# Kernel optimization log

Measured on AMD Instinct MI355X. Metric: run time of the kernel, lower is better.

Reference implementation:

```python
import jax, jax.numpy as jnp
import numpy as np

H = 256  # hidden_size
E = 768  # embedding dim / lstm input size
V = 7987 # vocab
B = 256  # batch
T = 512  # seq len


def setup_inputs() -> dict:
    key = jax.random.key(0)
    ks = jax.random.split(key, 12)
    s = 0.05
    return {
        "input_tensor": jax.random.randint(ks[0], (B, T), 0, V),
        "target_idx": jax.random.randint(ks[1], (B,), 0, T),
        "max_length": T,
        "emb": jax.random.normal(ks[2], (V, E), dtype=jnp.float32),
        "w_ih_f": jax.random.normal(ks[3], (4 * H, E), dtype=jnp.float32) * s,
        "w_hh_f": jax.random.normal(ks[4], (4 * H, H), dtype=jnp.float32) * s,
        "b_ih_f": jax.random.normal(ks[5], (4 * H,), dtype=jnp.float32) * s,
        "b_hh_f": jax.random.normal(ks[6], (4 * H,), dtype=jnp.float32) * s,
        "w_ih_b": jax.random.normal(ks[7], (4 * H, E), dtype=jnp.float32) * s,
        "w_hh_b": jax.random.normal(ks[8], (4 * H, H), dtype=jnp.float32) * s,
        "b_ih_b": jax.random.normal(ks[9], (4 * H,), dtype=jnp.float32) * s,
        "b_hh_b": jax.random.normal(ks[10], (4 * H,), dtype=jnp.float32) * s,
        "w_out": jax.random.normal(ks[11], (1, 2 * H), dtype=jnp.float32) * s,
        "b_out": jnp.zeros((1,), dtype=jnp.float32),
    }


def _lstm_cell(x, h, c, w_ih, w_hh, b):
    # PyTorch gate order: i, f, g, o
    gates = x @ w_ih.T + h @ w_hh.T + b  # [B, 4H]
    i, f, g, o = jnp.split(gates, 4, axis=-1)
    c_new = jax.nn.sigmoid(f) * c + jax.nn.sigmoid(i) * jnp.tanh(g)
    h_new = jax.nn.sigmoid(o) * jnp.tanh(c_new)
    return h_new, c_new


def reference(input_tensor, target_idx, max_length, emb,
              w_ih_f, w_hh_f, b_ih_f, b_hh_f,
              w_ih_b, w_hh_b, b_ih_b, b_hh_b,
              w_out, b_out):
    bsz = input_tensor.shape[0]
    # embed whole sequence up front: [T, B, E]
    xs = jnp.transpose(emb[input_tensor], (1, 0, 2))
    bf = b_ih_f + b_hh_f
    bb = b_ih_b + b_hh_b
    h0 = jnp.zeros((bsz, H), dtype=xs.dtype)
    init = (h0, h0, h0, h0)

    # NOTE: original calls bidirectional LSTM one step at a time carrying state,
    # so BOTH directions run forward in time (backward dir just uses reverse weights).
    def step(carry, x):
        hf, cf, hb, cb = carry
        hf, cf = _lstm_cell(x, hf, cf, w_ih_f, w_hh_f, bf)
        hb, cb = _lstm_cell(x, hb, cb, w_ih_b, w_hh_b, bb)
        return (hf, cf, hb, cb), jnp.concatenate([hf, hb], axis=-1)

    _, encoder_outputs = jax.lax.scan(step, init, xs)  # [T, B, 2H]
    # gather hidden state at each example's target index
    gathered = encoder_outputs[target_idx, jnp.arange(bsz)]  # [B, 2H]
    out = jax.nn.sigmoid(gathered @ w_out.T + b_out)  # [B, 1]
    return out[:, None, :]  # [B, 1, 1] matching torch output shape
```

## Files before the change

kernel.cpp:

```cpp
#include <hip/hip_runtime.h>
#include <hip/hip_bf16.h>

#define Bx 256
#define Tx 512
#define Ex 768
#define Hx 256
#define Gx 1024
#define Vx 7987

typedef unsigned short u16;
typedef unsigned int u32;
typedef __bf16 bf16;
typedef bf16 bf16x8 __attribute__((ext_vector_type(8)));
typedef u16 u16x8 __attribute__((ext_vector_type(8)));
typedef float f32x4 __attribute__((ext_vector_type(4)));
typedef int i32x4 __attribute__((ext_vector_type(4)));

__device__ __forceinline__ u16 f2bf(float f) {
  union { float f; u32 u; } x; x.f = f;
  u32 r = x.u + 0x7fffu + ((x.u >> 16) & 1u);
  return (u16)(r >> 16);
}
__device__ __forceinline__ float bf2f(u16 b) {
  union { u32 u; float f; } x; x.u = ((u32)b) << 16;
  return x.f;
}
__device__ __forceinline__ void gload16(const void* g, void* l) {
  __builtin_amdgcn_global_load_lds((const __attribute__((address_space(1))) u32*)g,
                                   (__attribute__((address_space(3))) u32*)l, 16, 0, 0);
}
__device__ __forceinline__ float sigf(float x) {
  return __builtin_amdgcn_rcpf(1.f + __builtin_amdgcn_exp2f(x * -1.442695041f));
}
__device__ __forceinline__ void bar_ds() {
  __builtin_amdgcn_sched_barrier(0);
  asm volatile("s_waitcnt lgkmcnt(0)" ::: "memory");
  __builtin_amdgcn_s_barrier();
  __builtin_amdgcn_sched_barrier(0);
}
#define WAITV(N) { asm volatile("s_waitcnt vmcnt(" #N ")"); __builtin_amdgcn_sched_barrier(0); }

__device__ __forceinline__ void gld8u(u16x8& d, const u16* base, u32 voff) {
  asm volatile("global_load_dwordx4 %0, %1, %2" : "=&v"(d) : "v"(voff), "s"(base));
}
__device__ __forceinline__ void mfma_i8(i32x4& d, i32x4 a, i32x4 b) {
  asm volatile("v_mfma_i32_16x16x64_i8 %0, %1, %2, %0" : "+v"(d) : "v"(a), "a"(b));
}


__global__ void k_cvt(const float* __restrict__ src, u16* __restrict__ dst, int n) {
  int i = blockIdx.x * blockDim.x + threadIdx.x;
  int st = gridDim.x * blockDim.x;
  for (; i < n; i += st) dst[i] = f2bf(src[i]);
}

__global__ void k_bias(const float* __restrict__ bihf, const float* __restrict__ bhhf,
                       const float* __restrict__ bihb, const float* __restrict__ bhhb,
                       float* __restrict__ bcat) {
  int i = blockIdx.x * blockDim.x + threadIdx.x;
  if (i < Gx) { bcat[i] = bihf[i] + bhhf[i]; bcat[Gx + i] = bihb[i] + bhhb[i]; }
}

__global__ void k_scales(const float* __restrict__ wf, const float* __restrict__ wb,
                         float* __restrict__ s) {
  int row = blockIdx.x;
  const float* w = (row < Gx) ? (wf + (size_t)row * Hx) : (wb + (size_t)(row - Gx) * Hx);
  int l = threadIdx.x;
  float m = 0.f;
  for (int j = l; j < Hx; j += 64) m = fmaxf(m, fabsf(w[j]));
#pragma unroll
  for (int off = 32; off; off >>= 1) m = fmaxf(m, __shfl_down(m, off));
  if (l == 0) s[row] = fmaxf(m, 1e-20f) * (1.f / 127.f);
}

__global__ void k_pack_i8(const float* __restrict__ wf, const float* __restrict__ wb,
                          const float* __restrict__ s, char* __restrict__ pk) {
  int i = blockIdx.x * 256 + threadIdx.x;
  int lane = i & 63, nb = (i >> 6) & 63, kc = (i >> 12) & 3, dir = (i >> 14) & 1;
  int n = nb * 16 + (lane & 15);
  int k0 = kc * 64 + ((lane >> 4) << 4);
  const float* w = dir ? wb : wf;
  float inv = 1.f / s[dir * Gx + n];
  int dw[4];
#pragma unroll
  for (int d4 = 0; d4 < 4; ++d4) {
    int v = 0;
#pragma unroll
    for (int j = 0; j < 4; ++j) {
      int q = (int)rintf(w[(size_t)n * Hx + k0 + d4 * 4 + j] * inv);
      v |= (q & 255) << (8 * j);
    }
    dw[d4] = v;
  }
  *(int4*)(pk + (size_t)i * 16) = make_int4(dw[0], dw[1], dw[2], dw[3]);
}

__global__ __launch_bounds__(256) void k_vproj(
    const u16* __restrict__ embbf, const u16* __restrict__ wih,
    const float* __restrict__ bcat, u16* __restrict__ vp) {
  __shared__ u16 sA[128 * 64];
  __shared__ u16 sB[128 * 64];
  const int tid = threadIdx.x;
  const int l = tid & 63, w = tid >> 6;
  const int bx = blockIdx.x & 15, by = blockIdx.x >> 4;
  const int wm = w >> 1, wn = w & 1;
  const int lr = l >> 3, lc = l & 7;

  f32x4 acc[4][4];
#pragma unroll
  for (int a = 0; a < 4; ++a)
#pragma unroll
    for (int b = 0; b < 4; ++b) acc[a][b] = f32x4{0.f, 0.f, 0.f, 0.f};

  size_t asrc[4], bsrc[4];
#pragma unroll
  for (int j = 0; j < 4; ++j) {
    int row = j * 32 + w * 8 + lr;
    int m = by * 128 + row;
    int er = (m < Vx) ? m : 0;
    asrc[j] = (size_t)er * (Ex * 2) + (size_t)((lc * 16) ^ ((row & 7) << 4));
    bsrc[j] = (size_t)(bx * 128 + row) * (Ex * 2) + (size_t)((lc * 16) ^ ((row & 7) << 4));
  }

  for (int kt = 0; kt < 12; ++kt) {
    const char* ebase = (const char*)embbf + (size_t)kt * 128;
    const char* wbase = (const char*)wih + (size_t)kt * 128;
#pragma unroll
    for (int j = 0; j < 4; ++j) {
      gload16(ebase + asrc[j], (char*)sA + (j * 32 + w * 8) * 128);
      gload16(wbase + bsrc[j], (char*)sB + (j * 32 + w * 8) * 128);
    }
    __syncthreads();
#pragma unroll
    for (int kk = 0; kk < 2; ++kk) {
      int kb = kk * 64 + ((l >> 4) * 16);
      bf16x8 av[4], bv[4];
#pragma unroll
      for (int f = 0; f < 4; ++f) {
        int r = wm * 64 + f * 16 + (l & 15);
        av[f] = *(const bf16x8*)((const char*)sA + r * 128 + (kb ^ ((r & 7) << 4)));
      }
#pragma unroll
      for (int f = 0; f < 4; ++f) {
        int n = wn * 64 + f * 16 + (l & 15);
        bv[f] = *(const bf16x8*)((const char*)sB + n * 128 + (kb ^ ((n & 7) << 4)));
      }
#pragma unroll
      for (int fm = 0; fm < 4; ++fm)
#pragma unroll
        for (int fn = 0; fn < 4; ++fn)
          acc[fm][fn] = __builtin_amdgcn_mfma_f32_16x16x32_bf16(av[fm], bv[fn], acc[fm][fn], 0, 0, 0);
    }
    __syncthreads();
  }
#pragma unroll
  for (int fn = 0; fn < 4; ++fn) {
    int col = bx * 128 + wn * 64 + fn * 16 + (l & 15);
    int dirc = col >> 10, c10 = col & 1023;
    int gq = c10 >> 8, wq = (c10 >> 5) & 7, fcq = (c10 >> 4) & 1, uq = c10 & 15;
    int pos = (wq * 16 + uq) * 8 + gq * 2 + fcq;
    float bias = bcat[col];
#pragma unroll
    for (int fm = 0; fm < 4; ++fm) {
      int m0 = by * 128 + wm * 64 + fm * 16 + ((l >> 4) << 2);
#pragma unroll
      for (int r = 0; r < 4; ++r)
        vp[((size_t)(m0 + r) * 2 + dirc) * 1024 + pos] = f2bf(acc[fm][fn][r] + bias);
    }
  }
}

#define STEPI(T, RB, WB, XC) {                                                \
  i32x4 acc[8];                                                               \
  _Pragma("unroll") for (int nt = 0; nt < 8; ++nt) acc[nt] = i32x4{0, 0, 0, 0}; \
  _Pragma("unroll") for (int kc = 0; kc < 4; ++kc) {                          \
    i32x4 a = *(const i32x4*)((RB) + kc * 1024 + aoff);                       \
    _Pragma("unroll") for (int nt = 0; nt < 8; ++nt)                          \
      mfma_i8(acc[nt], a, wres[kc][nt]);                                      \
  }                                                                           \
  asm volatile("s_nop 7\n\ts_nop 7");                                         \
  float ga[2][4];                                                             \
  _Pragma("unroll") for (int fc = 0; fc < 2; ++fc)                            \
    _Pragma("unroll") for (int g = 0; g < 4; ++g)                             \
      ga[fc][g] = (float)acc[g * 2 + fc][0] * qs[g * 2 + fc]                  \
                  + bf2f(XC[g * 2 + fc]);                                     \
  _Pragma("unroll") for (int fc = 0; fc < 2; ++fc) {                          \
    float si = sigf(ga[fc][0]);                                               \
    float sf = sigf(ga[fc][1]);                                               \
    float tv = 2.f * sigf(2.f * ga[fc][2]) - 1.f;                             \
    float so = sigf(ga[fc][3]);                                               \
    float cn = sf * creg[fc] + si * tv;                                       \
    float hn = so * (2.f * sigf(2.f * cn) - 1.f);                             \
    creg[fc] = cn;                                                            \
    if ((T) == tgt)                                                           \
      gath[(size_t)(b0 + q) * 512 + dir * 256 + w * 32 + fc * 16 + c] = hn;   \
    int qh = (int)rintf(hn * 127.f);                                          \
    _Pragma("unroll") for (int m = 0; m < 4; ++m)                             \
      *((WB) + wb_base + fc * 256 + m * 64 + (((q - m) & 3) << 4)) = (char)qh; \
  }                                                                           \
  bar_ds();                                                                   \
}

__global__ __launch_bounds__(512, 2) void k_rnn(
    const char* __restrict__ wq, const float* __restrict__ wsc,
    const u16* __restrict__ vp, const int* __restrict__ input,
    const int* __restrict__ target, float* __restrict__ gath) {
  __shared__ __align__(16) char shd[2][4096];
  __shared__ int stok[2048];
  const int tid = threadIdx.x;
  const int l = tid & 63, w = tid >> 6;
  const int q = l >> 4, c = l & 15;
  const int dir = blockIdx.x >> 6, slice = blockIdx.x & 63;
  const int b0 = slice * 4;
  const char* wqd = wq + (size_t)dir * 262144;

  i32x4 wres[4][8];
#pragma unroll
  for (int kc = 0; kc < 4; ++kc)
#pragma unroll
    for (int nt = 0; nt < 8; ++nt) {
      int nb = (nt >> 1) * 16 + w * 2 + (nt & 1);
      wres[kc][nt] = *(const i32x4*)(wqd + ((size_t)(kc * 64 + nb) * 64 + l) * 16);
    }
  float qs[8];
#pragma unroll
  for (int nt = 0; nt < 8; ++nt)
    qs[nt] = wsc[dir * Gx + (nt >> 1) * 256 + w * 32 + (nt & 1) * 16 + c] * (1.f / 127.f);

  for (int i = tid; i < 2048; i += 512)
    stok[i] = input[(b0 + (i >> 9)) * Tx + (i & 511)];
  for (int i = tid; i < 2048; i += 512) ((int*)shd)[i] = 0;

  float creg[2] = {0.f, 0.f};
  const int tgt = target[b0 + q];
  const u32 go2 = (u32)((w * 16 + c) * 16 + dir * 2048);
  const int tk0 = input[(b0 + q) * Tx + 0];
  const int tk1 = input[(b0 + q) * Tx + 1];

  const int aoff = (q << 8) + (c << 4);
  const int wb_base = (w >> 1) * 1024 + (w & 1) * 512 + c;
  const char* rb0 = &shd[0][0];
  const char* rb1 = &shd[1][0];
  char* wb0 = &shd[0][0];
  char* wb1 = &shd[1][0];

  __syncthreads();
  asm volatile("s_waitcnt vmcnt(0)" ::: "memory");
  __builtin_amdgcn_sched_barrier(0);

  u16x8 xvA, xvB;
  gld8u(xvA, vp, (u32)tk0 * 4096 + go2);
  gld8u(xvB, vp, (u32)tk1 * 4096 + go2);

#pragma unroll 1
  for (int t = 0; t < Tx; t += 2) {
    WAITV(0);
    u16x8 xcA = xvA, xcB = xvB;
    int ta = stok[q * 512 + ((t + 2 < Tx) ? t + 2 : Tx - 1)];
    int tb = stok[q * 512 + ((t + 3 < Tx) ? t + 3 : Tx - 1)];
    gld8u(xvA, vp, (u32)ta * 4096 + go2);
    gld8u(xvB, vp, (u32)tb * 4096 + go2);
    STEPI(t, rb0, wb1, xcA);
    STEPI(t + 1, rb1, wb0, xcB);
  }
}

__global__ void k_out(const float* __restrict__ gath, const float* __restrict__ wout,
                      const float* __restrict__ bout, float* __restrict__ out) {
  int b = blockIdx.x, l = threadIdx.x;
  float s = 0.f;
  for (int j = l; j < 512; j += 64) s += gath[(size_t)b * 512 + j] * wout[j];
#pragma unroll
  for (int off = 32; off; off >>= 1) s += __shfl_down(s, off);
  if (l == 0) out[b] = 1.f / (1.f + __expf(-(s + bout[0])));
}

extern "C" void kernel_launch(void* const* d_in, const int* in_sizes, int n_in,
                              void* d_out, int out_size, void* d_ws, size_t ws_size,
                              hipStream_t stream) {
  const int* input = (const int*)d_in[0];
  const int* target = (const int*)d_in[1];
  const float* emb  = (const float*)d_in[3];
  const float* wihf = (const float*)d_in[4];
  const float* whhf = (const float*)d_in[5];
  const float* bihf = (const float*)d_in[6];
  const float* bhhf = (const float*)d_in[7];
  const float* wihb = (const float*)d_in[8];
  const float* whhb = (const float*)d_in[9];
  const float* bihb = (const float*)d_in[10];
  const float* bhhb = (const float*)d_in[11];
  const float* wout = (const float*)d_in[12];
  const float* bout = (const float*)d_in[13];
  float* out = (float*)d_out;

  char* ws = (char*)d_ws;
  u16* embbf  = (u16*)(ws + 0);
  u16* wih    = (u16*)(ws + 12268032);
  char* wq    = (char*)(ws + 15413760);
  float* wsc  = (float*)(ws + 15938048);
  float* bcat = (float*)(ws + 15946240);
  float* gath = (float*)(ws + 15954432);
  u16* vp     = (u16*)(ws + 16478720);

  k_cvt<<<1024, 256, 0, stream>>>(emb, embbf, Vx * Ex);
  k_cvt<<<512, 256, 0, stream>>>(wihf, wih, Gx * Ex);
  k_cvt<<<512, 256, 0, stream>>>(wihb, wih + Gx * Ex, Gx * Ex);
  k_bias<<<4, 256, 0, stream>>>(bihf, bhhf, bihb, bhhb, bcat);
  k_scales<<<2048, 64, 0, stream>>>(whhf, whhb, wsc);
  k_pack_i8<<<128, 256, 0, stream>>>(whhf, whhb, wsc, wq);
  k_vproj<<<1008, 256, 0, stream>>>(embbf, wih, bcat, vp);
  k_rnn<<<128, 512, 0, stream>>>(wq, wsc, vp, input, target, gath);
  k_out<<<256, 64, 0, stream>>>(gath, wout, bout, out);
}
```

Before: 589.3 us.

## Quantize vocab input projections to int8 and halve batch per recurrent block

Measured after the change: 651.2 us. +10.5%, slower.

```diff
diff --git a/kernel.cpp b/kernel.cpp
--- a/kernel.cpp
+++ b/kernel.cpp
@@ -40,8 +40,8 @@
 }
 #define WAITV(N) { asm volatile("s_waitcnt vmcnt(" #N ")"); __builtin_amdgcn_sched_barrier(0); }
 
-__device__ __forceinline__ void gld8u(u16x8& d, const u16* base, u32 voff) {
-  asm volatile("global_load_dwordx4 %0, %1, %2" : "=&v"(d) : "v"(voff), "s"(base));
+__device__ __forceinline__ void gld2(int2& d, const char* base, u32 voff) {
+  asm volatile("global_load_dwordx2 %0, %1, %2" : "=&v"(d) : "v"(voff), "s"(base));
 }
 __device__ __forceinline__ void mfma_i8(i32x4& d, i32x4 a, i32x4 b) {
   asm volatile("v_mfma_i32_16x16x64_i8 %0, %1, %2, %0" : "+v"(d) : "v"(a), "a"(b));
@@ -170,7 +170,44 @@
   }
 }
 
-#define STEPI(T, RB, WB, XC) {                                                \
+__global__ __launch_bounds__(512) void k_vq(u16* __restrict__ vp, float* __restrict__ scg) {
+  const int tid = threadIdx.x;
+  const int l = tid & 63;
+  int row = blockIdx.x * 8 + (tid >> 6);
+  bool valid = row < 2 * Vx;
+  int rr = valid ? row : 2 * Vx - 1;
+  const u16* src = vp + (size_t)rr * 1024;
+  float v[16];
+  float m = 0.f;
+#pragma unroll
+  for (int j = 0; j < 16; ++j) {
+    v[j] = bf2f(src[l * 16 + j]);
+    m = fmaxf(m, fabsf(v[j]));
+  }
+#pragma unroll
+  for (int off = 32; off; off >>= 1) m = fmaxf(m, __shfl_xor(m, off));
+  float sc = fmaxf(m, 1e-20f) * (1.f / 127.f);
+  float inv = 1.f / sc;
+  if (valid && l == 0) scg[row] = sc;
+  __syncthreads();
+  if (valid) {
+    int dw[4];
+#pragma unroll
+    for (int d4 = 0; d4 < 4; ++d4) {
+      int wv = 0;
+#pragma unroll
+      for (int j = 0; j < 4; ++j) {
+        int qv = (int)rintf(v[d4 * 4 + j] * inv);
+        wv |= (qv & 255) << (8 * j);
+      }
+      dw[d4] = wv;
+    }
+    char* dst = (char*)vp + (size_t)blockIdx.x * 16384 + (size_t)(row & 7) * 1024;
+    *(int4*)(dst + l * 16) = make_int4(dw[0], dw[1], dw[2], dw[3]);
+  }
+}
+
+#define STEPI(T, RB, WB, XC, SC) {                                            \
   i32x4 acc[8];                                                               \
   _Pragma("unroll") for (int nt = 0; nt < 8; ++nt) acc[nt] = i32x4{0, 0, 0, 0}; \
   _Pragma("unroll") for (int kc = 0; kc < 4; ++kc) {                          \
@@ -181,9 +218,12 @@
   asm volatile("s_nop 7\n\ts_nop 7");                                         \
   float ga[2][4];                                                             \
   _Pragma("unroll") for (int fc = 0; fc < 2; ++fc)                            \
-    _Pragma("unroll") for (int g = 0; g < 4; ++g)                             \
-      ga[fc][g] = (float)acc[g * 2 + fc][0] * qs[g * 2 + fc]                  \
-                  + bf2f(XC[g * 2 + fc]);                                     \
+    _Pragma("unroll") for (int g = 0; g < 4; ++g) {                           \
+      int j = g * 2 + fc;                                                     \
+      int wd = (j < 4) ? (XC).x : (XC).y;                                     \
+      float xval = (float)((wd << (24 - 8 * (j & 3))) >> 24) * (SC);          \
+      ga[fc][g] = (float)acc[j][0] * qs[j] + xval;                            \
+    }                                                                         \
   _Pragma("unroll") for (int fc = 0; fc < 2; ++fc) {                          \
     float si = sigf(ga[fc][0]);                                               \
     float sf = sigf(ga[fc][1]);                                               \
@@ -192,26 +232,28 @@
     float cn = sf * creg[fc] + si * tv;                                       \
     float hn = so * (2.f * sigf(2.f * cn) - 1.f);                             \
     creg[fc] = cn;                                                            \
-    if ((T) == tgt)                                                           \
-      gath[(size_t)(b0 + q) * 512 + dir * 256 + w * 32 + fc * 16 + c] = hn;   \
+    if ((T) == tgt && q < 2)                                                  \
+      gath[(size_t)(b0 + (q & 1)) * 512 + dir * 256 + w * 32 + fc * 16 + c] = hn; \
     int qh = (int)rintf(hn * 127.f);                                          \
     _Pragma("unroll") for (int m = 0; m < 4; ++m)                             \
-      *((WB) + wb_base + fc * 256 + m * 64 + (((q - m) & 3) << 4)) = (char)qh; \
+      *((WB) + wb_base + fc * 256 + m * 16) = (char)qh;                       \
   }                                                                           \
   bar_ds();                                                                   \
 }
 
 __global__ __launch_bounds__(512, 2) void k_rnn(
     const char* __restrict__ wq, const float* __restrict__ wsc,
-    const u16* __restrict__ vp, const int* __restrict__ input,
-    const int* __restrict__ target, float* __restrict__ gath) {
+    const char* __restrict__ vpq, const float* __restrict__ scg,
+    const int* __restrict__ input, const int* __restrict__ target,
+    float* __restrict__ gath) {
   __shared__ __align__(16) char shd[2][4096];
-  __shared__ int stok[2048];
+  __shared__ int stok[1024];
+  __shared__ float ssc[Vx];
   const int tid = threadIdx.x;
   const int l = tid & 63, w = tid >> 6;
   const int q = l >> 4, c = l & 15;
-  const int dir = blockIdx.x >> 6, slice = blockIdx.x & 63;
-  const int b0 = slice * 4;
+  const int dir = blockIdx.x >> 7, slice = blockIdx.x & 127;
+  const int b0 = slice * 2;
   const char* wqd = wq + (size_t)dir * 262144;
 
   i32x4 wres[4][8];
@@ -227,18 +269,17 @@
   for (int nt = 0; nt < 8; ++nt)
     qs[nt] = wsc[dir * Gx + (nt >> 1) * 256 + w * 32 + (nt & 1) * 16 + c] * (1.f / 127.f);
 
-  for (int i = tid; i < 2048; i += 512)
+  for (int i = tid; i < 1024; i += 512)
     stok[i] = input[(b0 + (i >> 9)) * Tx + (i & 511)];
+  for (int i = tid; i < Vx; i += 512) ssc[i] = scg[i * 2 + dir];
   for (int i = tid; i < 2048; i += 512) ((int*)shd)[i] = 0;
 
   float creg[2] = {0.f, 0.f};
-  const int tgt = target[b0 + q];
-  const u32 go2 = (u32)((w * 16 + c) * 16 + dir * 2048);
-  const int tk0 = input[(b0 + q) * Tx + 0];
-  const int tk1 = input[(b0 + q) * Tx + 1];
+  const int tgt = target[b0 + (q & 1)];
+  const u32 go2 = (u32)((w * 16 + c) * 8);
 
   const int aoff = (q << 8) + (c << 4);
-  const int wb_base = (w >> 1) * 1024 + (w & 1) * 512 + c;
+  const int wb_base = (w >> 1) * 1024 + (w & 1) * 512 + (q << 6) + c;
   const char* rb0 = &shd[0][0];
   const char* rb1 = &shd[1][0];
   char* wb0 = &shd[0][0];
@@ -248,20 +289,32 @@
   asm volatile("s_waitcnt vmcnt(0)" ::: "memory");
   __builtin_amdgcn_sched_barrier(0);
 
-  u16x8 xvA, xvB;
-  gld8u(xvA, vp, (u32)tk0 * 4096 + go2);
-  gld8u(xvB, vp, (u32)tk1 * 4096 + go2);
+  int tk0 = stok[(q & 1) * 512 + 0];
+  int tk1 = stok[(q & 1) * 512 + 1];
+  float scA = ssc[tk0], scB = ssc[tk1];
+  int2 xvA, xvB;
+  {
+    u32 rA = (u32)(tk0 * 2 + dir), rB = (u32)(tk1 * 2 + dir);
+    gld2(xvA, vpq, ((rA >> 3) << 14) + ((rA & 7) << 10) + go2);
+    gld2(xvB, vpq, ((rB >> 3) << 14) + ((rB & 7) << 10) + go2);
+  }
 
 #pragma unroll 1
   for (int t = 0; t < Tx; t += 2) {
     WAITV(0);
-    u16x8 xcA = xvA, xcB = xvB;
-    int ta = stok[q * 512 + ((t + 2 < Tx) ? t + 2 : Tx - 1)];
-    int tb = stok[q * 512 + ((t + 3 < Tx) ? t + 3 : Tx - 1)];
-    gld8u(xvA, vp, (u32)ta * 4096 + go2);
-    gld8u(xvB, vp, (u32)tb * 4096 + go2);
-    STEPI(t, rb0, wb1, xcA);
-    STEPI(t + 1, rb1, wb0, xcB);
+    int2 xcA = xvA, xcB = xvB;
+    float cA = scA, cB = scB;
+    int ta = stok[(q & 1) * 512 + ((t + 2 < Tx) ? t + 2 : Tx - 1)];
+    int tb = stok[(q & 1) * 512 + ((t + 3 < Tx) ? t + 3 : Tx - 1)];
+    scA = ssc[ta];
+    scB = ssc[tb];
+    {
+      u32 rA = (u32)(ta * 2 + dir), rB = (u32)(tb * 2 + dir);
+      gld2(xvA, vpq, ((rA >> 3) << 14) + ((rA & 7) << 10) + go2);
+      gld2(xvB, vpq, ((rB >> 3) << 14) + ((rB & 7) << 10) + go2);
+    }
+    STEPI(t, rb0, wb1, xcA, cA);
+    STEPI(t + 1, rb1, wb0, xcB, cB);
   }
 }
 
@@ -301,6 +354,7 @@
   float* bcat = (float*)(ws + 15946240);
   float* gath = (float*)(ws + 15954432);
   u16* vp     = (u16*)(ws + 16478720);
+  float* scg  = (float*)(ws + 49508864);
 
   k_cvt<<<1024, 256, 0, stream>>>(emb, embbf, Vx * Ex);
   k_cvt<<<512, 256, 0, stream>>>(wihf, wih, Gx * Ex);
@@ -309,6 +363,7 @@
   k_scales<<<2048, 64, 0, stream>>>(whhf, whhb, wsc);
   k_pack_i8<<<128, 256, 0, stream>>>(whhf, whhb, wsc, wq);
   k_vproj<<<1008, 256, 0, stream>>>(embbf, wih, bcat, vp);
-  k_rnn<<<128, 512, 0, stream>>>(wq, wsc, vp, input, target, gath);
+  k_vq<<<(2 * Vx + 7) / 8, 512, 0, stream>>>(vp, scg);
+  k_rnn<<<256, 512, 0, stream>>>(wq, wsc, (const char*)vp, scg, input, target, gath);
   k_out<<<256, 64, 0, stream>>>(gath, wout, bout, out);
 }
```

## Double RNN block to 1024 threads, halving per-wave gate columns

Applied to the files above, without the earlier changes.

After: 488.9 us. 1.21x faster.

```diff
diff --git a/kernel.cpp b/kernel.cpp
--- a/kernel.cpp
+++ b/kernel.cpp
@@ -12,7 +12,6 @@
 typedef unsigned int u32;
 typedef __bf16 bf16;
 typedef bf16 bf16x8 __attribute__((ext_vector_type(8)));
-typedef u16 u16x8 __attribute__((ext_vector_type(8)));
 typedef float f32x4 __attribute__((ext_vector_type(4)));
 typedef int i32x4 __attribute__((ext_vector_type(4)));
 
@@ -24,6 +23,9 @@
 __device__ __forceinline__ float bf2f(u16 b) {
   union { u32 u; float f; } x; x.u = ((u32)b) << 16;
   return x.f;
+}
+__device__ __forceinline__ float asf(u32 u) {
+  union { u32 u; float f; } x; x.u = u; return x.f;
 }
 __device__ __forceinline__ void gload16(const void* g, void* l) {
   __builtin_amdgcn_global_load_lds((const __attribute__((address_space(1))) u32*)g,
@@ -40,11 +42,14 @@
 }
 #define WAITV(N) { asm volatile("s_waitcnt vmcnt(" #N ")"); __builtin_amdgcn_sched_barrier(0); }
 
-__device__ __forceinline__ void gld8u(u16x8& d, const u16* base, u32 voff) {
-  asm volatile("global_load_dwordx4 %0, %1, %2" : "=&v"(d) : "v"(voff), "s"(base));
+__device__ __forceinline__ void gld2(int2& d, const char* base, u32 voff) {
+  asm volatile("global_load_dwordx2 %0, %1, %2" : "=&v"(d) : "v"(voff), "s"(base));
 }
 __device__ __forceinline__ void mfma_i8(i32x4& d, i32x4 a, i32x4 b) {
   asm volatile("v_mfma_i32_16x16x64_i8 %0, %1, %2, %0" : "+v"(d) : "v"(a), "a"(b));
+}
+__device__ __forceinline__ void mfma_i8z(i32x4& d, i32x4 a, i32x4 b) {
+  asm volatile("v_mfma_i32_16x16x64_i8 %0, %1, %2, 0" : "=&v"(d) : "v"(a), "a"(b));
 }
 
 
@@ -157,8 +162,8 @@
   for (int fn = 0; fn < 4; ++fn) {
     int col = bx * 128 + wn * 64 + fn * 16 + (l & 15);
     int dirc = col >> 10, c10 = col & 1023;
-    int gq = c10 >> 8, wq = (c10 >> 5) & 7, fcq = (c10 >> 4) & 1, uq = c10 & 15;
-    int pos = (wq * 16 + uq) * 8 + gq * 2 + fcq;
+    int gq = c10 >> 8, uq = c10 & 255;
+    int pos = uq * 4 + gq;
     float bias = bcat[col];
 #pragma unroll
     for (int fm = 0; fm < 4; ++fm) {
@@ -170,43 +175,55 @@
   }
 }
 
-#define STEPI(T, RB, WB, XC) {                                                \
-  i32x4 acc[8];                                                               \
-  _Pragma("unroll") for (int nt = 0; nt < 8; ++nt) acc[nt] = i32x4{0, 0, 0, 0}; \
-  _Pragma("unroll") for (int kc = 0; kc < 4; ++kc) {                          \
-    i32x4 a = *(const i32x4*)((RB) + kc * 1024 + aoff);                       \
-    _Pragma("unroll") for (int nt = 0; nt < 8; ++nt)                          \
-      mfma_i8(acc[nt], a, wres[kc][nt]);                                      \
-  }                                                                           \
-  asm volatile("s_nop 7\n\ts_nop 7");                                         \
-  float ga[2][4];                                                             \
-  _Pragma("unroll") for (int fc = 0; fc < 2; ++fc)                            \
-    _Pragma("unroll") for (int g = 0; g < 4; ++g)                             \
-      ga[fc][g] = (float)acc[g * 2 + fc][0] * qs[g * 2 + fc]                  \
-                  + bf2f(XC[g * 2 + fc]);                                     \
-  _Pragma("unroll") for (int fc = 0; fc < 2; ++fc) {                          \
-    float si = sigf(ga[fc][0]);                                               \
-    float sf = sigf(ga[fc][1]);                                               \
-    float tv = 2.f * sigf(2.f * ga[fc][2]) - 1.f;                             \
-    float so = sigf(ga[fc][3]);                                               \
-    float cn = sf * creg[fc] + si * tv;                                       \
-    float hn = so * (2.f * sigf(2.f * cn) - 1.f);                             \
-    creg[fc] = cn;                                                            \
-    if ((T) == tgt)                                                           \
-      gath[(size_t)(b0 + q) * 512 + dir * 256 + w * 32 + fc * 16 + c] = hn;   \
-    int qh = (int)rintf(hn * 127.f);                                          \
-    _Pragma("unroll") for (int m = 0; m < 4; ++m)                             \
-      *((WB) + wb_base + fc * 256 + m * 64 + (((q - m) & 3) << 4)) = (char)qh; \
-  }                                                                           \
-  bar_ds();                                                                   \
-}
-
-__global__ __launch_bounds__(512, 2) void k_rnn(
+#define STEPB(T, RB, WB, XC) {                                               \
+  i32x4 a0 = *(const i32x4*)(RB);                                            \
+  i32x4 a1 = *(const i32x4*)((RB) + 1024);                                   \
+  i32x4 a2 = *(const i32x4*)((RB) + 2048);                                   \
+  i32x4 a3 = *(const i32x4*)((RB) + 3072);                                   \
+  i32x4 acc0, acc1, acc2, acc3;                                              \
+  mfma_i8z(acc0, a0, wres[0][0]);                                            \
+  mfma_i8z(acc1, a0, wres[0][1]);                                            \
+  mfma_i8z(acc2, a0, wres[0][2]);                                            \
+  mfma_i8z(acc3, a0, wres[0][3]);                                            \
+  mfma_i8(acc0, a1, wres[1][0]);                                             \
+  mfma_i8(acc1, a1, wres[1][1]);                                             \
+  mfma_i8(acc2, a1, wres[1][2]);                                             \
+  mfma_i8(acc3, a1, wres[1][3]);                                             \
+  mfma_i8(acc0, a2, wres[2][0]);                                             \
+  mfma_i8(acc1, a2, wres[2][1]);                                             \
+  mfma_i8(acc2, a2, wres[2][2]);                                             \
+  mfma_i8(acc3, a2, wres[2][3]);                                             \
+  mfma_i8(acc0, a3, wres[3][0]);                                             \
+  mfma_i8(acc1, a3, wres[3][1]);                                             \
+  mfma_i8(acc2, a3, wres[3][2]);                                             \
+  mfma_i8(acc3, a3, wres[3][3]);                                             \
+  asm volatile("s_nop 7\n\ts_nop 7");                                        \
+  float g0 = (float)acc0[0] * qs[0] + asf(((u32)(XC).x) << 16);              \
+  float g1 = (float)acc1[0] * qs[1] + asf(((u32)(XC).x) & 0xffff0000u);      \
+  float g2 = (float)acc2[0] * qs[2] + asf(((u32)(XC).y) << 16);              \
+  float g3 = (float)acc3[0] * qs[3] + asf(((u32)(XC).y) & 0xffff0000u);      \
+  float si = sigf(g0);                                                       \
+  float sf = sigf(g1);                                                       \
+  float tv = 2.f * sigf(2.f * g2) - 1.f;                                     \
+  float so = sigf(g3);                                                       \
+  float cn = sf * creg + si * tv;                                            \
+  float hn = so * (2.f * sigf(2.f * cn) - 1.f);                              \
+  creg = cn;                                                                 \
+  if ((T) == tgt) gath[(size_t)(b0 + q) * 512 + dir * 256 + w * 16 + c] = hn; \
+  int qh = (int)rintf(hn * 127.f);                                           \
+  *((WB) + wp0) = (char)qh;                                                  \
+  *((WB) + wp1) = (char)qh;                                                  \
+  *((WB) + wp2) = (char)qh;                                                  \
+  *((WB) + wp3) = (char)qh;                                                  \
+  bar_ds();                                                                  \
+}
+
+__global__ __launch_bounds__(1024, 4) void k_rnn(
     const char* __restrict__ wq, const float* __restrict__ wsc,
-    const u16* __restrict__ vp, const int* __restrict__ input,
+    const char* __restrict__ vp, const int* __restrict__ input,
     const int* __restrict__ target, float* __restrict__ gath) {
   __shared__ __align__(16) char shd[2][4096];
-  __shared__ int stok[2048];
+  __shared__ int stok[4 * 520];
   const int tid = threadIdx.x;
   const int l = tid & 63, w = tid >> 6;
   const int q = l >> 4, c = l & 15;
@@ -214,54 +231,55 @@
   const int b0 = slice * 4;
   const char* wqd = wq + (size_t)dir * 262144;
 
-  i32x4 wres[4][8];
+  i32x4 wres[4][4];
 #pragma unroll
   for (int kc = 0; kc < 4; ++kc)
 #pragma unroll
-    for (int nt = 0; nt < 8; ++nt) {
-      int nb = (nt >> 1) * 16 + w * 2 + (nt & 1);
-      wres[kc][nt] = *(const i32x4*)(wqd + ((size_t)(kc * 64 + nb) * 64 + l) * 16);
-    }
-  float qs[8];
-#pragma unroll
-  for (int nt = 0; nt < 8; ++nt)
-    qs[nt] = wsc[dir * Gx + (nt >> 1) * 256 + w * 32 + (nt & 1) * 16 + c] * (1.f / 127.f);
-
-  for (int i = tid; i < 2048; i += 512)
-    stok[i] = input[(b0 + (i >> 9)) * Tx + (i & 511)];
-  for (int i = tid; i < 2048; i += 512) ((int*)shd)[i] = 0;
-
-  float creg[2] = {0.f, 0.f};
+    for (int g = 0; g < 4; ++g)
+      wres[kc][g] = *(const i32x4*)(wqd + ((size_t)(kc * 64 + g * 16 + w) * 64 + l) * 16);
+  float qs[4];
+#pragma unroll
+  for (int g = 0; g < 4; ++g)
+    qs[g] = wsc[dir * Gx + g * 256 + w * 16 + c] * (1.f / 127.f);
+
+  for (int i = tid; i < 4 * 520; i += 1024) {
+    int r = i / 520, t = i - r * 520;
+    stok[i] = input[(b0 + r) * Tx + (t < Tx ? t : Tx - 1)];
+  }
+  for (int i = tid; i < 2048; i += 1024) ((int*)shd)[i] = 0;
+
+  float creg = 0.f;
   const int tgt = target[b0 + q];
-  const u32 go2 = (u32)((w * 16 + c) * 16 + dir * 2048);
-  const int tk0 = input[(b0 + q) * Tx + 0];
-  const int tk1 = input[(b0 + q) * Tx + 1];
+  const u32 go2 = (u32)(dir * 2048 + (w * 16 + c) * 8);
 
   const int aoff = (q << 8) + (c << 4);
-  const int wb_base = (w >> 1) * 1024 + (w & 1) * 512 + c;
-  const char* rb0 = &shd[0][0];
-  const char* rb1 = &shd[1][0];
-  char* wb0 = &shd[0][0];
-  char* wb1 = &shd[1][0];
+  const char* rb0 = &shd[0][0] + aoff;
+  const char* rb1 = &shd[1][0] + aoff;
+  const int wbs = (w >> 2) * 1024 + (w & 3) * 256 + c;
+  char* wb0 = &shd[0][0] + wbs;
+  char* wb1 = &shd[1][0] + wbs;
+  const int wp0 = ((q - 0) & 3) << 4;
+  const int wp1 = 64 + (((q - 1) & 3) << 4);
+  const int wp2 = 128 + (((q - 2) & 3) << 4);
+  const int wp3 = 192 + (((q - 3) & 3) << 4);
+  const int* stq = stok + q * 520;
 
   __syncthreads();
   asm volatile("s_waitcnt vmcnt(0)" ::: "memory");
   __builtin_amdgcn_sched_barrier(0);
 
-  u16x8 xvA, xvB;
-  gld8u(xvA, vp, (u32)tk0 * 4096 + go2);
-  gld8u(xvB, vp, (u32)tk1 * 4096 + go2);
+  int2 xvA, xvB;
+  gld2(xvA, vp, (u32)stq[0] * 4096 + go2);
+  gld2(xvB, vp, (u32)stq[1] * 4096 + go2);
 
 #pragma unroll 1
   for (int t = 0; t < Tx; t += 2) {
     WAITV(0);
-    u16x8 xcA = xvA, xcB = xvB;
-    int ta = stok[q * 512 + ((t + 2 < Tx) ? t + 2 : Tx - 1)];
-    int tb = stok[q * 512 + ((t + 3 < Tx) ? t + 3 : Tx - 1)];
-    gld8u(xvA, vp, (u32)ta * 4096 + go2);
-    gld8u(xvB, vp, (u32)tb * 4096 + go2);
-    STEPI(t, rb0, wb1, xcA);
-    STEPI(t + 1, rb1, wb0, xcB);
+    int2 xcA = xvA, xcB = xvB;
+    gld2(xvA, vp, (u32)stq[t + 2] * 4096 + go2);
+    gld2(xvB, vp, (u32)stq[t + 3] * 4096 + go2);
+    STEPB(t, rb0, wb1, xcA);
+    STEPB(t + 1, rb1, wb0, xcB);
   }
 }
 
@@ -309,6 +327,6 @@
   k_scales<<<2048, 64, 0, stream>>>(whhf, whhb, wsc);
   k_pack_i8<<<128, 256, 0, stream>>>(whhf, whhb, wsc, wq);
   k_vproj<<<1008, 256, 0, stream>>>(embbf, wih, bcat, vp);
-  k_rnn<<<128, 512, 0, stream>>>(wq, wsc, vp, input, target, gath);
+  k_rnn<<<128, 1024, 0, stream>>>(wq, wsc, (const char*)vp, input, target, gath);
   k_out<<<256, 64, 0, stream>>>(gath, wout, bout, out);
 }
```
